# Performance work log

Measured on AMD Instinct MI355X. Metric: run time of the kernel, lower is better.

Reference implementation:

```python
import jax, jax.numpy as jnp
import numpy as np
from jax import lax

HUMAN_CONF = 0.7
IOU_TH = 0.5


def setup_inputs() -> dict:
    key = jax.random.key(0)
    k1, k2 = jax.random.split(key)
    B, Q, C = 16, 2048, 2
    return {
        "human_logits": jax.random.normal(k1, (B, Q, C), dtype=jnp.float32),
        "pred_boxes": jax.random.uniform(k2, (B, Q, 4), dtype=jnp.float32),  # cxcywh in [0,1]
        "img_h": 800,
        "img_w": 1333,
    }


def box_cxcywh_to_xyxy(b):
    cx, cy, w, h = b[..., 0], b[..., 1], b[..., 2], b[..., 3]
    return jnp.stack([cx - 0.5 * w, cy - 0.5 * h, cx + 0.5 * w, cy + 0.5 * h], axis=-1)


def pairwise_iou(b):
    # b: [Q,4] xyxy -> iou: [Q,Q]
    area = jnp.clip(b[:, 2] - b[:, 0], 0) * jnp.clip(b[:, 3] - b[:, 1], 0)
    lt = jnp.maximum(b[:, None, :2], b[None, :, :2])
    rb = jnp.minimum(b[:, None, 2:], b[None, :, 2:])
    wh = jnp.clip(rb - lt, 0)
    inter = wh[..., 0] * wh[..., 1]
    union = area[:, None] + area[None, :] - inter
    return inter / jnp.maximum(union, 1e-9)


def nms_keep(boxes, scores, valid, iou_th):
    # Greedy NMS on one image with fixed shapes; returns keep mask [Q].
    Q = scores.shape[0]
    order = jnp.argsort(jnp.where(valid, -scores, jnp.inf))  # valid boxes first, score desc
    b = boxes[order]
    v = valid[order]
    iou = pairwise_iou(b)                       # [Q,Q]
    idx = jnp.arange(Q)
    sup_mat = (iou > iou_th) & (idx[None, :] > idx[:, None])  # i suppresses later j

    def step(supp, i):
        keep_i = v[i] & jnp.logical_not(supp[i])
        supp = supp | (keep_i & sup_mat[i])
        return supp, keep_i

    _, keep_sorted = lax.scan(step, jnp.zeros(Q, bool), idx)
    return jnp.zeros(Q, bool).at[order].set(keep_sorted)


def reference(human_logits, pred_boxes, img_h, img_w):
    prob = jax.nn.softmax(human_logits, axis=-1)          # [B,Q,C]
    scores = prob.max(axis=-1)                            # [B,Q]
    labels = prob.argmax(axis=-1)                         # [B,Q]
    boxes = box_cxcywh_to_xyxy(pred_boxes)                # [B,Q,4]
    scale = jnp.array([img_w, img_h, img_w, img_h], dtype=boxes.dtype)
    boxes = boxes * scale
    valid = (labels == 0) & (scores >= HUMAN_CONF)
    keep = jax.vmap(lambda b, s, v: nms_keep(b, s, v, IOU_TH))(boxes, scores, valid)
    scores_out = jnp.where(keep, scores, 0.0)
    boxes_out = jnp.where(keep[..., None], boxes, 0.0).astype(jnp.int32)
    return scores_out, boxes_out, keep
```

## Files before the change

kernel.cpp:

```cpp
#include <hip/hip_runtime.h>
#include <math.h>


#define QN     2048
#define NS     1024
#define NSLICE 16
#define MATW   17408
#define MAGIC  0x5ca1ab1eu

__device__ __forceinline__ int rb32(int wb) { return 64 * wb * (33 - wb); }

__device__ __forceinline__ unsigned long long shfl_xor_u64(unsigned long long x, int m) {
    int lo = __shfl_xor((int)(unsigned)(x & 0xffffffffull), m, 64);
    int hi = __shfl_xor((int)(unsigned)(x >> 32), m, 64);
    return ((unsigned long long)(unsigned)hi << 32) | (unsigned)lo;
}

__device__ __forceinline__ unsigned long long score_key(float2 l, int q, bool* valid_out) {
    float mx = fmaxf(l.x, l.y), mn = fminf(l.x, l.y);
    float e = expf(mn - mx);
    float score = 1.0f / (1.0f + e);
    bool valid = (l.x >= l.y) && (score >= 0.7f);
    *valid_out = valid;
    unsigned sbits = valid ? __float_as_uint(score) : 0u;
    return ((unsigned long long)(~sbits) << 32) | (unsigned)q;
}

#define SCAN_LOAD(RBUF, DIAG, c) do {                                         \
    const int wb_ = (c) >> 1, rl_ = 32 - 2 * wb_;                             \
    const int half_ = ((c) & 1) << 5;                                         \
    const int Lc_ = min(max((int)(tid & 31), 2 * wb_), 31);                   \
    const int rb0_ = rb32(wb_) + half_ * rl_ + (Lc_ - 2 * wb_);               \
    _Pragma("unroll")                                                         \
    for (int t = 0; t < 16; ++t) RBUF[t] = gm[rb0_ + (tb + t) * rl_];         \
    DIAG = gm[rb32(wb_) + (half_ + lam) * rl_ + ((c) - 2 * wb_)];             \
} while (0)

#define SCAN_PROC(RBUF, DIAG, c) do {                                         \
    int lim_ = min(32, Ms - ((c) << 5));                                      \
    unsigned limmask_ = (lim_ >= 32) ? 0xFFFFFFFFu : ((1u << lim_) - 1u);     \
    unsigned rw_ = ((unsigned)__builtin_amdgcn_readlane((int)rem, (c)))       \
                   | ~limmask_;                                               \
    unsigned keepmask_ = 0;                                                   \
    _Pragma("unroll")                                                         \
    for (int t = 0; t < 32; ++t) {                                            \
        unsigned keep_ = ((~rw_) >> t) & 1u;                                  \
        unsigned rword_ = (unsigned)__builtin_amdgcn_readlane((int)(DIAG), t);\
        rw_ |= (0u - keep_) & rword_;                                         \
        keepmask_ |= keep_ << t;                                              \
    }                                                                         \
    unsigned part_ = 0;                                                       \
    _Pragma("unroll")                                                         \
    for (int t = 0; t < 16; ++t)                                              \
        part_ |= (0u - ((keepmask_ >> (tb + t)) & 1u)) & RBUF[t];             \
    part_ |= (unsigned)__shfl_xor((int)part_, 32, 64);                        \
    rem |= part_;                                                             \
    if (tid == 0) skm[(c)] = keepmask_;                                       \
} while (0)

__global__ __launch_bounds__(1024) void kfused(
    const float* __restrict__ logits, const float* __restrict__ pboxes,
    const int* __restrict__ img_h_p, const int* __restrict__ img_w_p,
    unsigned* __restrict__ wflag, unsigned* __restrict__ wmat,
    float* __restrict__ out, int B)
{
    __shared__ __align__(16) char smem[110848];
    unsigned long long* skey = (unsigned long long*)smem;
    float* sx1 = (float*)(smem + 8192);
    float* sy1 = (float*)(smem + 12288);
    float* sx2 = (float*)(smem + 16384);
    float* sy2 = (float*)(smem + 20480);
    float* sar = (float*)(smem + 24576);
    unsigned short* sidxl = (unsigned short*)(smem + 28672);
    int* sMp = (int*)(smem + 32896);
    unsigned long long* skeyB = (unsigned long long*)(smem + 33024);
    unsigned* skm = (unsigned*)(smem + 33024);
    unsigned* smat = (unsigned*)(smem + 41216);

    const int blk = blockIdx.x;
    const int b = blk % B, slice = blk / B;
    const int tid = threadIdx.x, lane = tid & 63, wave = tid >> 6;
    const float sw = (float)(*img_w_p), sh = (float)(*img_h_p);
    const long BQ = (long)B * QN;

    if (tid == 0) *sMp = 0;
    __syncthreads();

    const unsigned long long lmask_lt = (1ull << lane) - 1ull;
#pragma unroll
    for (int qq = 0; qq < 2; ++qq) {
        int q = tid + qq * 1024;
        float2 l = ((const float2*)logits)[b * QN + q];
        bool valid;
        unsigned long long key = score_key(l, q, &valid);
        unsigned long long mb = __ballot(valid);
        int base = 0;
        if (lane == 0 && mb) base = atomicAdd(sMp, __popcll(mb));
        base = __shfl(base, 0, 64);
        if (valid) {
            int slot = base + __popcll(mb & lmask_lt);
            if (slot < NS) skey[slot] = key;
        }
    }
    __syncthreads();
    const int M = *sMp;

    if (M <= NS) {
        unsigned long long v = (tid < M) ? skey[tid] : ~0ull;
        __syncthreads();
#pragma unroll
        for (int k = 2; k <= 64; k <<= 1) {
            bool dir = ((tid & k) == 0);
#pragma unroll
            for (int j = k >> 1; j > 0; j >>= 1) {
                unsigned long long o = shfl_xor_u64(v, j);
                bool takeMin = (dir == ((tid & j) == 0));
                v = ((v < o) == takeMin) ? v : o;
            }
        }
        int pp = 0;
        for (int k = 128; k <= NS; k <<= 1) {
            bool dir = ((tid & k) == 0);
            for (int j = k >> 1; j >= 64; j >>= 1) {
                unsigned long long* buf = pp ? skeyB : skey;
                pp ^= 1;
                buf[tid] = v;
                __syncthreads();
                unsigned long long o = buf[tid ^ j];
                bool takeMin = (dir == ((tid & j) == 0));
                v = ((v < o) == takeMin) ? v : o;
            }
#pragma unroll
            for (int j = 32; j > 0; j >>= 1) {
                unsigned long long o = shfl_xor_u64(v, j);
                bool takeMin = (dir == ((tid & j) == 0));
                v = ((v < o) == takeMin) ? v : o;
            }
        }
        int qi = (int)((unsigned)v & 0xffffu);
        sidxl[tid] = (unsigned short)qi;
        float x1 = 0.f, y1 = 0.f, x2 = 0.f, y2 = 0.f, ar = 0.f;
        if (tid < M) {
            float4 pb = ((const float4*)pboxes)[b * QN + qi];
            x1 = (pb.x - 0.5f * pb.z) * sw;
            y1 = (pb.y - 0.5f * pb.w) * sh;
            x2 = (pb.x + 0.5f * pb.z) * sw;
            y2 = (pb.y + 0.5f * pb.w) * sh;
            ar = fmaxf(x2 - x1, 0.f) * fmaxf(y2 - y1, 0.f);
        }
        sx1[tid] = x1; sy1[tid] = y1; sx2[tid] = x2; sy2[tid] = y2; sar[tid] = ar;
        __syncthreads();

        unsigned* mat = wmat + (long)b * MATW;
        const int NG = (M + 3) >> 2;
        const int W64 = (M + 63) >> 6;
        for (int gi = slice + 16 * wave; gi < NG; gi += 256) {
            const int g = gi << 2;
            const int nr = min(4, M - g);
            const int wb = g >> 6;
            const int rl = 32 - 2 * wb;
            float ax1[4], ay1[4], ax2[4], ay2[4], aar[4];
            int rbase[4];
#pragma unroll
            for (int r = 0; r < 4; ++r) {
                int i = g + min(r, nr - 1);
                ax1[r] = sx1[i]; ay1[r] = sy1[i];
                ax2[r] = sx2[i]; ay2[r] = sy2[i]; aar[r] = sar[i];
                rbase[r] = rb32(wb) + ((g + r) & 63) * rl;
            }
            for (int w = wb; w < W64; ++w) {
                int j = (w << 6) | lane;
                float bx1 = sx1[j], by1 = sy1[j], bx2 = sx2[j], by2 = sy2[j], bar = sar[j];
#pragma unroll
                for (int r = 0; r < 4; ++r) {
                    float ltx = fmaxf(ax1[r], bx1), lty = fmaxf(ay1[r], by1);
                    float rbx = fminf(ax2[r], bx2), rby = fminf(ay2[r], by2);
                    float wx = fmaxf(rbx - ltx, 0.f), wy = fmaxf(rby - lty, 0.f);
                    float inter = wx * wy;
                    float uni = aar[r] + bar - inter;
                    float iou = inter / fmaxf(uni, 1e-9f);
                    bool sup = (iou > 0.5f) && (j > g + r);
                    unsigned long long bal = __ballot(sup);
                    if (lane == 0 && r < nr)
                        *(unsigned long long*)(mat + rbase[r] + 2 * (w - wb)) = bal;
                }
            }
        }
    }

    if (tid < 128) {
        int q = slice * 128 + tid;
        int base = b * QN + q;
        out[base] = 0.f;
        out[BQ * 5 + base] = 0.f;
        float4 z; z.x = 0.f; z.y = 0.f; z.z = 0.f; z.w = 0.f;
        ((float4*)(out + BQ))[base] = z;
    }

    __syncthreads();
    if (tid == 0)
        __hip_atomic_store(&wflag[b * NSLICE + slice], MAGIC,
                           __ATOMIC_RELEASE, __HIP_MEMORY_SCOPE_AGENT);
    if (slice != 0) return;

    if (wave == 0) {
        const unsigned* fp = &wflag[b * NSLICE + (lane & (NSLICE - 1))];
        for (;;) {
            unsigned f = (lane < NSLICE)
                ? __hip_atomic_load(fp, __ATOMIC_ACQUIRE, __HIP_MEMORY_SCOPE_AGENT)
                : MAGIC;
            if (__all(f == MAGIC)) break;
            __builtin_amdgcn_s_sleep(2);
        }
    }
    __syncthreads();

    if (M <= NS) {
        const int W64 = (M + 63) >> 6;
        const int nw4 = rb32(W64) >> 2;
        const uint4* gm4 = (const uint4*)(wmat + (long)b * MATW);
        uint4* sm4 = (uint4*)smat;
        for (int i = tid; i < nw4; i += 1024) sm4[i] = gm4[i];
        __syncthreads();

        if (tid < 64) {
            const unsigned* gm = smat;
            unsigned rem = 0;
            const int Ms = __builtin_amdgcn_readfirstlane(M);
            const int C = (Ms + 31) >> 5;
            const int lam = min(tid, 31);
            const int tb = (tid >> 5) << 4;
            unsigned rA[16], rB[16], diagA = 0, diagB = 0;
            if (C > 0) SCAN_LOAD(rA, diagA, 0);
            for (int c = 0; c < C; c += 2) {
                if (c + 1 < C) SCAN_LOAD(rB, diagB, c + 1);
                SCAN_PROC(rA, diagA, c);
                if (c + 1 < C) {
                    if (c + 2 < C) SCAN_LOAD(rA, diagA, c + 2);
                    SCAN_PROC(rB, diagB, c + 1);
                }
            }
        }
        __syncthreads();

        for (int s = tid; s < M; s += 1024) {
            if ((skm[s >> 5] >> (s & 31)) & 1u) {
                int qi = sidxl[s];
                int base = b * QN + qi;
                float2 l = ((const float2*)logits)[base];
                float e = expf(fminf(l.x, l.y) - fmaxf(l.x, l.y));
                float score = 1.0f / (1.0f + e);
                float4 pb = ((const float4*)pboxes)[base];
                float x1 = (pb.x - 0.5f * pb.z) * sw, y1 = (pb.y - 0.5f * pb.w) * sh;
                float x2 = (pb.x + 0.5f * pb.z) * sw, y2 = (pb.y + 0.5f * pb.w) * sh;
                out[base] = score;
                out[BQ * 5 + base] = 1.f;
                float4 ob;
                ob.x = truncf(x1); ob.y = truncf(y1);
                ob.z = truncf(x2); ob.w = truncf(y2);
                ((float4*)(out + BQ))[base] = ob;
            }
        }
    } else {
        unsigned long long* skeyF = (unsigned long long*)smem;
        unsigned char* ssupp = (unsigned char*)(smem + 16384);
        unsigned char* keepqF = (unsigned char*)(smem + 18432);
        for (int qq = tid; qq < QN; qq += 1024) {
            float2 l = ((const float2*)logits)[b * QN + qq];
            bool valid;
            skeyF[qq] = score_key(l, qq, &valid);
        }
        keepqF[tid] = 0; keepqF[tid + 1024] = 0;
        __syncthreads();
        for (int k = 2; k <= QN; k <<= 1)
            for (int j = k >> 1; j > 0; j >>= 1) {
                int i = ((tid & ~(j - 1)) << 1) | (tid & (j - 1));
                int p = i | j;
                bool up = ((i & k) == 0);
                unsigned long long a = skeyF[i], c2 = skeyF[p];
                if ((a > c2) == up) { skeyF[i] = c2; skeyF[p] = a; }
                __syncthreads();
            }
        for (int s = tid; s < M; s += 1024) ssupp[s] = 0;
        __syncthreads();
        for (int i = 0; i < M; ++i) {
            __syncthreads();
            if (ssupp[i]) continue;
            int ia = (unsigned short)(unsigned)skeyF[i];
            float4 pa = ((const float4*)pboxes)[b * QN + ia];
            float ax1 = (pa.x - 0.5f * pa.z) * sw, ay1 = (pa.y - 0.5f * pa.w) * sh;
            float ax2 = (pa.x + 0.5f * pa.z) * sw, ay2 = (pa.y + 0.5f * pa.w) * sh;
            float areaA = fmaxf(ax2 - ax1, 0.f) * fmaxf(ay2 - ay1, 0.f);
            for (int jj = i + 1 + tid; jj < M; jj += 1024) {
                int jb = (unsigned short)(unsigned)skeyF[jj];
                float4 pq = ((const float4*)pboxes)[b * QN + jb];
                float bx1 = (pq.x - 0.5f * pq.z) * sw, by1 = (pq.y - 0.5f * pq.w) * sh;
                float bx2 = (pq.x + 0.5f * pq.z) * sw, by2 = (pq.y + 0.5f * pq.w) * sh;
                float ltx = fmaxf(ax1, bx1), lty = fmaxf(ay1, by1);
                float rbx = fminf(ax2, bx2), rby = fminf(ay2, by2);
                float wx = fmaxf(rbx - ltx, 0.f), wy = fmaxf(rby - lty, 0.f);
                float inter = wx * wy;
                float areaB = fmaxf(bx2 - bx1, 0.f) * fmaxf(by2 - by1, 0.f);
                float uni = areaA + areaB - inter;
                if (inter / fmaxf(uni, 1e-9f) > 0.5f) ssupp[jj] = 1;
            }
        }
        __syncthreads();
        for (int s = tid; s < M; s += 1024)
            if (!ssupp[s]) keepqF[(unsigned short)(unsigned)skeyF[s]] = 1;
        __syncthreads();
#pragma unroll
        for (int qq = 0; qq < 2; ++qq) {
            int q = tid + qq * 1024;
            int base = b * QN + q;
            float2 l = ((const float2*)logits)[base];
            float e = expf(fminf(l.x, l.y) - fmaxf(l.x, l.y));
            float score = 1.0f / (1.0f + e);
            float4 pb = ((const float4*)pboxes)[base];
            float x1 = (pb.x - 0.5f * pb.z) * sw, y1 = (pb.y - 0.5f * pb.w) * sh;
            float x2 = (pb.x + 0.5f * pb.z) * sw, y2 = (pb.y + 0.5f * pb.w) * sh;
            int kp = keepqF[q];
            out[base] = kp ? score : 0.f;
            out[BQ * 5 + base] = kp ? 1.f : 0.f;
            float4 ob;
            ob.x = kp ? truncf(x1) : 0.f;
            ob.y = kp ? truncf(y1) : 0.f;
            ob.z = kp ? truncf(x2) : 0.f;
            ob.w = kp ? truncf(y2) : 0.f;
            ((float4*)(out + BQ))[base] = ob;
        }
    }
}

extern "C" void kernel_launch(void* const* d_in, const int* in_sizes, int n_in,
                              void* d_out, int out_size, void* d_ws, size_t ws_size,
                              hipStream_t stream) {
    const float* logits = (const float*)d_in[0];
    const float* pboxes = (const float*)d_in[1];
    const int*   img_h  = (const int*)d_in[2];
    const int*   img_w  = (const int*)d_in[3];
    float* out = (float*)d_out;
    const int B = in_sizes[0] / (QN * 2);

    char* ws = (char*)d_ws;
    unsigned* wflag = (unsigned*)(ws + 0);
    unsigned* wmat  = (unsigned*)(ws + 1024);

    kfused<<<dim3(B * NSLICE), dim3(1024), 0, stream>>>(logits, pboxes, img_h, img_w,
                                                        wflag, wmat, out, B);
}
```

Baseline: 95.47 us.

## Keep sorted keys and boxes in registers; scan suppression matrix from global memory

The finalizing block no longer stages the suppression matrix into LDS. The scan reads it directly from global memory, which cuts the shared allocation from about 110KB to 41KB. The output stage reuses per-thread registers (sorted key, index, decoded box) instead of re-reading logits and boxes and recomputing the softmax score. The score is recovered from the packed key bits. This trades the bulk LDS copy and its barrier for global-latency loads inside the serial scan, while the smaller LDS footprint may allow more occupancy.

```diff
diff --git a/kernel.cpp b/kernel.cpp
--- a/kernel.cpp
+++ b/kernel.cpp
@@ -64,24 +64,26 @@
     unsigned* __restrict__ wflag, unsigned* __restrict__ wmat,
     float* __restrict__ out, int B)
 {
-    __shared__ __align__(16) char smem[110848];
+    __shared__ __align__(16) char smem[41216];
     unsigned long long* skey = (unsigned long long*)smem;
     float* sx1 = (float*)(smem + 8192);
     float* sy1 = (float*)(smem + 12288);
     float* sx2 = (float*)(smem + 16384);
     float* sy2 = (float*)(smem + 20480);
     float* sar = (float*)(smem + 24576);
-    unsigned short* sidxl = (unsigned short*)(smem + 28672);
     int* sMp = (int*)(smem + 32896);
     unsigned long long* skeyB = (unsigned long long*)(smem + 33024);
     unsigned* skm = (unsigned*)(smem + 33024);
-    unsigned* smat = (unsigned*)(smem + 41216);
 
     const int blk = blockIdx.x;
     const int b = blk % B, slice = blk / B;
     const int tid = threadIdx.x, lane = tid & 63, wave = tid >> 6;
     const float sw = (float)(*img_w_p), sh = (float)(*img_h_p);
     const long BQ = (long)B * QN;
+
+    unsigned long long vkey = ~0ull;
+    int qi = 0;
+    float px1 = 0.f, py1 = 0.f, px2 = 0.f, py2 = 0.f;
 
     if (tid == 0) *sMp = 0;
     __syncthreads();
@@ -106,16 +108,16 @@
     const int M = *sMp;
 
     if (M <= NS) {
-        unsigned long long v = (tid < M) ? skey[tid] : ~0ull;
+        vkey = (tid < M) ? skey[tid] : ~0ull;
         __syncthreads();
 #pragma unroll
         for (int k = 2; k <= 64; k <<= 1) {
             bool dir = ((tid & k) == 0);
 #pragma unroll
             for (int j = k >> 1; j > 0; j >>= 1) {
-                unsigned long long o = shfl_xor_u64(v, j);
+                unsigned long long o = shfl_xor_u64(vkey, j);
                 bool takeMin = (dir == ((tid & j) == 0));
-                v = ((v < o) == takeMin) ? v : o;
+                vkey = ((vkey < o) == takeMin) ? vkey : o;
             }
         }
         int pp = 0;
@@ -124,31 +126,30 @@
             for (int j = k >> 1; j >= 64; j >>= 1) {
                 unsigned long long* buf = pp ? skeyB : skey;
                 pp ^= 1;
-                buf[tid] = v;
+                buf[tid] = vkey;
                 __syncthreads();
                 unsigned long long o = buf[tid ^ j];
                 bool takeMin = (dir == ((tid & j) == 0));
-                v = ((v < o) == takeMin) ? v : o;
+                vkey = ((vkey < o) == takeMin) ? vkey : o;
             }
 #pragma unroll
             for (int j = 32; j > 0; j >>= 1) {
-                unsigned long long o = shfl_xor_u64(v, j);
+                unsigned long long o = shfl_xor_u64(vkey, j);
                 bool takeMin = (dir == ((tid & j) == 0));
-                v = ((v < o) == takeMin) ? v : o;
-            }
-        }
-        int qi = (int)((unsigned)v & 0xffffu);
-        sidxl[tid] = (unsigned short)qi;
-        float x1 = 0.f, y1 = 0.f, x2 = 0.f, y2 = 0.f, ar = 0.f;
+                vkey = ((vkey < o) == takeMin) ? vkey : o;
+            }
+        }
+        qi = (int)((unsigned)vkey & 0xffffu);
+        float ar = 0.f;
         if (tid < M) {
             float4 pb = ((const float4*)pboxes)[b * QN + qi];
-            x1 = (pb.x - 0.5f * pb.z) * sw;
-            y1 = (pb.y - 0.5f * pb.w) * sh;
-            x2 = (pb.x + 0.5f * pb.z) * sw;
-            y2 = (pb.y + 0.5f * pb.w) * sh;
-            ar = fmaxf(x2 - x1, 0.f) * fmaxf(y2 - y1, 0.f);
-        }
-        sx1[tid] = x1; sy1[tid] = y1; sx2[tid] = x2; sy2[tid] = y2; sar[tid] = ar;
+            px1 = (pb.x - 0.5f * pb.z) * sw;
+            py1 = (pb.y - 0.5f * pb.w) * sh;
+            px2 = (pb.x + 0.5f * pb.z) * sw;
+            py2 = (pb.y + 0.5f * pb.w) * sh;
+            ar = fmaxf(px2 - px1, 0.f) * fmaxf(py2 - py1, 0.f);
+        }
+        sx1[tid] = px1; sy1[tid] = py1; sx2[tid] = px2; sy2[tid] = py2; sar[tid] = ar;
         __syncthreads();
 
         unsigned* mat = wmat + (long)b * MATW;
@@ -216,15 +217,8 @@
     __syncthreads();
 
     if (M <= NS) {
-        const int W64 = (M + 63) >> 6;
-        const int nw4 = rb32(W64) >> 2;
-        const uint4* gm4 = (const uint4*)(wmat + (long)b * MATW);
-        uint4* sm4 = (uint4*)smat;
-        for (int i = tid; i < nw4; i += 1024) sm4[i] = gm4[i];
-        __syncthreads();
-
         if (tid < 64) {
-            const unsigned* gm = smat;
+            const unsigned* gm = wmat + (long)b * MATW;
             unsigned rem = 0;
             const int Ms = __builtin_amdgcn_readfirstlane(M);
             const int C = (Ms + 31) >> 5;
@@ -243,23 +237,15 @@
         }
         __syncthreads();
 
-        for (int s = tid; s < M; s += 1024) {
-            if ((skm[s >> 5] >> (s & 31)) & 1u) {
-                int qi = sidxl[s];
-                int base = b * QN + qi;
-                float2 l = ((const float2*)logits)[base];
-                float e = expf(fminf(l.x, l.y) - fmaxf(l.x, l.y));
-                float score = 1.0f / (1.0f + e);
-                float4 pb = ((const float4*)pboxes)[base];
-                float x1 = (pb.x - 0.5f * pb.z) * sw, y1 = (pb.y - 0.5f * pb.w) * sh;
-                float x2 = (pb.x + 0.5f * pb.z) * sw, y2 = (pb.y + 0.5f * pb.w) * sh;
-                out[base] = score;
-                out[BQ * 5 + base] = 1.f;
-                float4 ob;
-                ob.x = truncf(x1); ob.y = truncf(y1);
-                ob.z = truncf(x2); ob.w = truncf(y2);
-                ((float4*)(out + BQ))[base] = ob;
-            }
+        if (tid < M && ((skm[tid >> 5] >> (tid & 31)) & 1u)) {
+            int base = b * QN + qi;
+            float score = __uint_as_float(~(unsigned)(vkey >> 32));
+            out[base] = score;
+            out[BQ * 5 + base] = 1.f;
+            float4 ob;
+            ob.x = truncf(px1); ob.y = truncf(py1);
+            ob.z = truncf(px2); ob.w = truncf(py2);
+            ((float4*)(out + BQ))[base] = ob;
         }
     } else {
         unsigned long long* skeyF = (unsigned long long*)smem;
```

Result: no change. 97.26 us (+1.9%).
